# Kernel optimization log

Measured on AMD Instinct MI355X. Metric: run time of the kernel, lower is better.

## Reference

```python
import jax, jax.numpy as jnp
import numpy as np

N, X_DIM, Y_DIM, HID = 8192, 512, 2048 // 4, 2048
Y_DIM = 512

def setup_inputs() -> dict:
    key = jax.random.key(0)
    ks = jax.random.split(key, 10)
    def lin(k, fan_in, fan_out):
        lim = 1.0 / np.sqrt(fan_in)
        kw, kb = jax.random.split(k)
        W = jax.random.uniform(kw, (fan_in, fan_out), jnp.float32, -lim, lim)
        b = jax.random.uniform(kb, (fan_out,), jnp.float32, -lim, lim)
        return W, b
    mu_W1, mu_b1 = lin(ks[0], X_DIM, HID)
    mu_W2, mu_b2 = lin(ks[1], HID, Y_DIM)
    lv_W1, lv_b1 = lin(ks[2], X_DIM, HID)
    lv_W2, lv_b2 = lin(ks[3], HID, Y_DIM)
    return {
        "x_samples": jax.random.normal(ks[4], (N, X_DIM), jnp.float32),
        "y_samples": jax.random.normal(ks[5], (N, Y_DIM), jnp.float32),
        "mu_W1": mu_W1, "mu_b1": mu_b1, "mu_W2": mu_W2, "mu_b2": mu_b2,
        "lv_W1": lv_W1, "lv_b1": lv_b1, "lv_W2": lv_W2, "lv_b2": lv_b2,
    }

def reference(x_samples, y_samples, mu_W1, mu_b1, mu_W2, mu_b2, lv_W1, lv_b1, lv_W2, lv_b2):
    # MLP heads (GEMMs)
    mu = jax.nn.relu(x_samples @ mu_W1 + mu_b1) @ mu_W2 + mu_b2          # [N, D]
    logvar = jnp.tanh(jax.nn.relu(x_samples @ lv_W1 + lv_b1) @ lv_W2 + lv_b2)  # [N, D]
    w = 0.5 * jnp.exp(-logvar)                                           # 1/(2*exp(logvar))
    n = x_samples.shape[0]

    # positive: -mean_i sum_d (mu_id - y_id)^2 * w_id
    positive = -(((mu - y_samples) ** 2) * w).sum(axis=1).mean()

    # negative (exact decomposition of the [N,N,D] broadcast):
    # -(1/N^2) sum_{i,d} w_id * (N*mu_id^2 - 2*mu_id*Sy_d + Sy2_d)
    Sy = y_samples.sum(axis=0)          # [D]
    Sy2 = (y_samples ** 2).sum(axis=0)  # [D]
    negative = -(w * (n * mu ** 2 - 2.0 * mu * Sy + Sy2)).sum() / (n * n)

    return positive - negative
```

## Files before the change

kernel.cpp:

```cpp
#include <hip/hip_runtime.h>
#include <hip/hip_bf16.h>
#include <stdint.h>

#define NS   8192
#define XD   512
#define HD   2048
#define YD   512

typedef unsigned short u16;
using bf16x8 = __attribute__((ext_vector_type(8))) short;
using f32x4  = __attribute__((ext_vector_type(4))) float;

__device__ __forceinline__ float bf2f(u16 u) {
  union { uint32_t i; float f; } v; v.i = ((uint32_t)u) << 16; return v.f;
}
__device__ __forceinline__ u16 f2b(float f) {
  __hip_bfloat16 hb = __float2bfloat16(f);
  return *(const u16*)&hb;
}
__device__ __forceinline__ float ld_in(const void* p, int f32, size_t i) {
  return f32 ? ((const float*)p)[i] : bf2f(((const u16*)p)[i]);
}
#define GLDS(gp, lp) __builtin_amdgcn_global_load_lds( \
    (__attribute__((address_space(1))) void*)(gp),     \
    (__attribute__((address_space(3))) void*)(lp), 16, 0, 0)

__device__ __forceinline__ int probe_f32(const void* p, int n_u16, int* sflag) {
  if (threadIdx.x == 0) *sflag = 0;
  __syncthreads();
  const u16* q = (const u16*)p;
  int wild = 0;
  for (int i = threadIdx.x; i < n_u16; i += blockDim.x) {
    float v = bf2f(q[i]);
    if (!(fabsf(v) <= 1000.0f)) wild = 1;
  }
  if (wild) *sflag = 1;
  __syncthreads();
  int r = *sflag;
  __syncthreads();
  return r;
}

__global__ __launch_bounds__(256) void prep_all(
    const void* __restrict__ x,
    const void* w1m, const void* b1m, const void* w2m, const void* b2m,
    const void* w1l, const void* b1l, const void* w2l, const void* b2l,
    u16* __restrict__ xb, float* __restrict__ biasv,
    u16* __restrict__ W1t, u16* __restrict__ W2tm, u16* __restrict__ W2tl) {
  __shared__ u16 tile[64 * 72];
  __shared__ int sflag;
  const int b = blockIdx.x;
  const int tid = threadIdx.x;

  if (b < 2048) {
    if (!probe_f32(x, 1024, &sflag)) return;
    const size_t base = (size_t)b * 2048 + (size_t)tid * 8;
    alignas(16) u16 o[8];
    const float4* s = (const float4*)((const float*)x + base);
    float4 v0 = s[0], v1 = s[1];
    o[0]=f2b(v0.x); o[1]=f2b(v0.y); o[2]=f2b(v0.z); o[3]=f2b(v0.w);
    o[4]=f2b(v1.x); o[5]=f2b(v1.y); o[6]=f2b(v1.z); o[7]=f2b(v1.w);
    *(uint4*)(xb + base) = *(const uint4*)o;
  } else if (b == 2048) {
    const int f3 = probe_f32(b1m, 1024, &sflag);
    const int f5 = probe_f32(b2m, 512, &sflag);
    const int f7 = probe_f32(b1l, 1024, &sflag);
    const int f9 = probe_f32(b2l, 512, &sflag);
    for (int i = tid; i < 5120; i += 256) {
      float v;
      if (i < 2048)      v = ld_in(b1m, f3, i);
      else if (i < 4096) v = ld_in(b1l, f7, i - 2048);
      else if (i < 4608) v = ld_in(b2m, f5, i - 4096);
      else               v = ld_in(b2l, f9, i - 4608);
      biasv[i] = v;
    }
  } else {
    const int id = b - 2049, which = id >> 8, t = id & 255;
    const void* in; u16* out; int R, C;
    if (which == 0)      { in = w1m; out = W1t;                   R = XD; C = HD; }
    else if (which == 1) { in = w2m; out = W2tm;                  R = HD; C = YD; }
    else if (which == 2) { in = w1l; out = W1t + (size_t)HD * XD; R = XD; C = HD; }
    else                 { in = w2l; out = W2tl;                  R = HD; C = YD; }
    const int f = probe_f32(in, 1024, &sflag);
    const int nbx = C >> 6;
    const int c0 = (t % nbx) * 64, r0 = (t / nbx) * 64;
    const int r = tid >> 2, cc = (tid & 3) * 16;
    if (f) {
      const float4* s = (const float4*)((const float*)in + (size_t)(r0 + r) * C + c0 + cc);
#pragma unroll
      for (int k = 0; k < 4; ++k) {
        float4 v = s[k];
        tile[r * 72 + cc + k * 4 + 0] = f2b(v.x);
        tile[r * 72 + cc + k * 4 + 1] = f2b(v.y);
        tile[r * 72 + cc + k * 4 + 2] = f2b(v.z);
        tile[r * 72 + cc + k * 4 + 3] = f2b(v.w);
      }
    } else {
      const uint4* s = (const uint4*)((const u16*)in + (size_t)(r0 + r) * C + c0 + cc);
      *(uint4*)&tile[r * 72 + cc]     = s[0];
      *(uint4*)&tile[r * 72 + cc + 8] = s[1];
    }
    __syncthreads();
    const int i = tid >> 2, jc = (tid & 3) * 16;
    alignas(16) u16 o[16];
#pragma unroll
    for (int j = 0; j < 16; ++j) o[j] = tile[(jc + j) * 72 + i];
    uint4* dq = (uint4*)&out[(size_t)(c0 + i) * R + r0 + jc];
    dq[0] = ((const uint4*)o)[0];
    dq[1] = ((const uint4*)o)[1];
  }
}

__global__ __launch_bounds__(256) void gemm1_kernel(
    const void* __restrict__ xraw, const u16* __restrict__ xb,
    const void* __restrict__ y,
    const u16* __restrict__ W1t,
    const float* __restrict__ bias,
    float* __restrict__ Sy, float* __restrict__ Sy2,
    u16* __restrict__ h_mu, u16* __restrict__ h_lv) {
  constexpr int K = XD;
  __shared__ alignas(16) u16 As[128 * 64];
  __shared__ alignas(16) u16 Bs[128 * 64];
  __shared__ int sflag;

  const int tid = threadIdx.x;

  if (blockIdx.x < 64) {
    const int yf = probe_f32(y, 1024, &sflag);
    const int half = tid >> 7;
    const int c0 = (tid & 127) * 4;
    const int r0 = blockIdx.x * 128 + half * 64;
    float s0 = 0.f, s1 = 0.f, s2 = 0.f, s3 = 0.f;
    float q0 = 0.f, q1 = 0.f, q2 = 0.f, q3 = 0.f;
    for (int r = r0; r < r0 + 64; r += 4) {
#pragma unroll
      for (int rr = 0; rr < 4; ++rr) {
        float v0, v1, v2, v3;
        if (yf) {
          const float4 t4 = *(const float4*)((const float*)y + (size_t)(r + rr) * YD + c0);
          v0 = t4.x; v1 = t4.y; v2 = t4.z; v3 = t4.w;
        } else {
          const uint2 t2 = *(const uint2*)((const u16*)y + (size_t)(r + rr) * YD + c0);
          v0 = bf2f((u16)(t2.x & 0xffff)); v1 = bf2f((u16)(t2.x >> 16));
          v2 = bf2f((u16)(t2.y & 0xffff)); v3 = bf2f((u16)(t2.y >> 16));
        }
        s0 += v0; q0 += v0 * v0;  s1 += v1; q1 += v1 * v1;
        s2 += v2; q2 += v2 * v2;  s3 += v3; q3 += v3 * v3;
      }
    }
    atomicAdd(&Sy[c0],     s0);  atomicAdd(&Sy2[c0],     q0);
    atomicAdd(&Sy[c0 + 1], s1);  atomicAdd(&Sy2[c0 + 1], q1);
    atomicAdd(&Sy[c0 + 2], s2);  atomicAdd(&Sy2[c0 + 2], q2);
    atomicAdd(&Sy[c0 + 3], s3);  atomicAdd(&Sy2[c0 + 3], q3);
    return;
  }

  const u16* A = probe_f32(xraw, 1024, &sflag) ? xb : (const u16*)xraw;

  const int wid = tid >> 6, lane = tid & 63;
  const int id = blockIdx.x - 64;
  const int xcd = id & 7, slot = id >> 3;
  const int m_idx = slot & 7;
  const int n_idx = slot >> 3;
  const int bm0 = (xcd * 8 + m_idx) * 128;
  const int bn0 = n_idx * 128;

  const int mrow = (wid >> 1) * 64, ncol = (wid & 1) * 64;
  const int quad = lane >> 4, c16 = lane & 15, cswz = c16 & 7;
  const int srow = lane >> 3, sc = lane & 7;
  const int scg  = (sc ^ srow) * 8;

  f32x4 acc[4][4] = {};

  for (int k0 = 0; k0 < K; k0 += 64) {
#pragma unroll
    for (int j = 0; j < 4; ++j) {
      const int grp = wid * 4 + j, row = grp * 8 + srow;
      GLDS(A   + (size_t)(bm0 + row) * K + (k0 + scg), As + grp * 512);
      GLDS(W1t + (size_t)(bn0 + row) * K + (k0 + scg), Bs + grp * 512);
    }
    __syncthreads();
#pragma unroll
    for (int h = 0; h < 2; ++h) {
      const int off = ((h * 4 + quad) ^ cswz) * 8;
      bf16x8 af[4], bfr[4];
#pragma unroll
      for (int mi = 0; mi < 4; ++mi)
        af[mi] = *(const bf16x8*)&As[(mrow + mi * 16 + c16) * 64 + off];
#pragma unroll
      for (int ni = 0; ni < 4; ++ni)
        bfr[ni] = *(const bf16x8*)&Bs[(ncol + ni * 16 + c16) * 64 + off];
#pragma unroll
      for (int mi = 0; mi < 4; ++mi)
#pragma unroll
        for (int ni = 0; ni < 4; ++ni)
          acc[mi][ni] = __builtin_amdgcn_mfma_f32_16x16x32_bf16(
              af[mi], bfr[ni], acc[mi][ni], 0, 0, 0);
    }
    __syncthreads();
  }

  const bool is_lv = bn0 >= HD;
  u16* dst = is_lv ? h_lv : h_mu;
  const int cb = bn0 - (is_lv ? HD : 0);
#pragma unroll
  for (int ni = 0; ni < 4; ++ni) {
    const int gc = ncol + ni * 16 + c16;
    const float bv = bias[bn0 + gc];
#pragma unroll
    for (int mi = 0; mi < 4; ++mi)
#pragma unroll
      for (int r = 0; r < 4; ++r) {
        const int grow = bm0 + mrow + mi * 16 + quad * 4 + r;
        dst[(size_t)grow * HD + (cb + gc)] = f2b(fmaxf(acc[mi][ni][r] + bv, 0.f));
      }
  }
}

__global__ __launch_bounds__(256) void gemm2_dual(
    const u16* __restrict__ hm, const u16* __restrict__ hl,
    const u16* __restrict__ W2m, const u16* __restrict__ W2l,
    const float* __restrict__ b2m, const float* __restrict__ b2l,
    const void* __restrict__ y,
    const float* __restrict__ Sy, const float* __restrict__ Sy2,
    double* __restrict__ gacc, unsigned* __restrict__ counter,
    float* __restrict__ out) {
  constexpr int K = HD;
  __shared__ alignas(16) u16 Am[64 * 64];
  __shared__ alignas(16) u16 Al[64 * 64];
  __shared__ alignas(16) u16 Bm[128 * 64];
  __shared__ alignas(16) u16 Bl[128 * 64];
  __shared__ double bs[4];
  __shared__ int sflag;

  const int yf = probe_f32(y, 1024, &sflag);

  const int tid = threadIdx.x, wid = tid >> 6, lane = tid & 63;
  const int MT = NS / 64, NT = YD / 128;
  const int id = blockIdx.x;
  const int xcd = id & 7, slot = id >> 3;
  const int bm0 = (xcd * (MT >> 3) + slot / NT) * 64;
  const int bn0 = (slot % NT) * 128;

  const int mrow = (wid >> 1) * 32, ncol = (wid & 1) * 64;
  const int quad = lane >> 4, c16 = lane & 15, cswz = c16 & 7;
  const int srow = lane >> 3, sc = lane & 7;
  const int scg  = (sc ^ srow) * 8;

  f32x4 am[2][4] = {}, al[2][4] = {};

  for (int k0 = 0; k0 < K; k0 += 64) {
#pragma unroll
    for (int j = 0; j < 2; ++j) {
      const int grp = wid * 2 + j, row = grp * 8 + srow;
      const size_t go = (size_t)(bm0 + row) * K + (k0 + scg);
      GLDS(hm + go, Am + grp * 512);
      GLDS(hl + go, Al + grp * 512);
    }
#pragma unroll
    for (int j = 0; j < 4; ++j) {
      const int grp = wid * 4 + j, row = grp * 8 + srow;
      const size_t go = (size_t)(bn0 + row) * K + (k0 + scg);
      GLDS(W2m + go, Bm + grp * 512);
      GLDS(W2l + go, Bl + grp * 512);
    }
    __syncthreads();
#pragma unroll
    for (int h = 0; h < 2; ++h) {
      const int off = ((h * 4 + quad) ^ cswz) * 8;
      bf16x8 afm[2], afl[2], bfm[4], bfl[4];
#pragma unroll
      for (int mi = 0; mi < 2; ++mi) {
        const int rl = (mrow + mi * 16 + c16) * 64 + off;
        afm[mi] = *(const bf16x8*)&Am[rl];
        afl[mi] = *(const bf16x8*)&Al[rl];
      }
#pragma unroll
      for (int ni = 0; ni < 4; ++ni) {
        const int rl = (ncol + ni * 16 + c16) * 64 + off;
        bfm[ni] = *(const bf16x8*)&Bm[rl];
        bfl[ni] = *(const bf16x8*)&Bl[rl];
      }
#pragma unroll
      for (int mi = 0; mi < 2; ++mi)
#pragma unroll
        for (int ni = 0; ni < 4; ++ni) {
          am[mi][ni] = __builtin_amdgcn_mfma_f32_16x16x32_bf16(
              afm[mi], bfm[ni], am[mi][ni], 0, 0, 0);
          al[mi][ni] = __builtin_amdgcn_mfma_f32_16x16x32_bf16(
              afl[mi], bfl[ni], al[mi][ni], 0, 0, 0);
        }
    }
    __syncthreads();
  }

  const float invN = 1.0f / (float)NS;
  float s = 0.f;
#pragma unroll
  for (int ni = 0; ni < 4; ++ni) {
    const int gcol = bn0 + ncol + ni * 16 + c16;
    const float bmv = b2m[gcol], blv = b2l[gcol];
    const float syv = Sy[gcol], sy2v = Sy2[gcol];
#pragma unroll
    for (int mi = 0; mi < 2; ++mi)
#pragma unroll
      for (int r = 0; r < 4; ++r) {
        const int grow = bm0 + mrow + mi * 16 + quad * 4 + r;
        const float m   = am[mi][ni][r] + bmv;
        const float lvp = al[mi][ni][r] + blv;
        const float w   = 0.5f * expf(-tanhf(lvp));
        const float yv  = ld_in(y, yf, (size_t)grow * YD + gcol);
        s += w * (yv * yv - 2.f * m * yv + (2.f * m * syv - sy2v) * invN);
      }
  }
  for (int off = 32; off > 0; off >>= 1) s += __shfl_down(s, off);
  if (lane == 0) bs[wid] = (double)s;
  __syncthreads();
  if (tid == 0) {
    atomicAdd(gacc, bs[0] + bs[1] + bs[2] + bs[3]);
    __threadfence();
    const unsigned old = atomicAdd(counter, 1u);
    if (old == gridDim.x - 1) {
      const double g = atomicAdd(gacc, 0.0);
      out[0] = (float)(-g / (double)NS);
    }
  }
}

extern "C" void kernel_launch(void* const* d_in, const int* in_sizes, int n_in,
                              void* d_out, int out_size, void* d_ws, size_t ws_size,
                              hipStream_t stream) {
  char* ws = (char*)d_ws;
  double*   gacc    = (double*)ws;
  unsigned* counter = (unsigned*)(ws + 8);
  float*    Sy      = (float*)(ws + 128);
  float*    Sy2     = (float*)(ws + 2176);
  float*    biasv   = (float*)(ws + 4224);
  u16* xb   = (u16*)(ws + 24704);
  u16* W1t  = xb + (size_t)NS * XD;
  u16* W2tm = W1t + (size_t)2 * HD * XD;
  u16* W2tl = W2tm + (size_t)YD * HD;
  u16* h_mu = W2tl + (size_t)YD * HD;
  u16* h_lv = h_mu + (size_t)NS * HD;

  hipMemsetAsync(d_ws, 0, 4224, stream);

  prep_all<<<2049 + 1024, 256, 0, stream>>>(
      d_in[0], d_in[2], d_in[3], d_in[4], d_in[5],
      d_in[6], d_in[7], d_in[8], d_in[9],
      xb, biasv, W1t, W2tm, W2tl);

  const float* b1  = biasv;
  const float* b2m = biasv + 4096, *b2l = biasv + 4608;

  gemm1_kernel<<<64 + (NS / 128) * ((2 * HD) / 128), 256, 0, stream>>>(
      d_in[0], xb, d_in[1], W1t, b1, Sy, Sy2, h_mu, h_lv);

  gemm2_dual<<<(NS / 64) * (YD / 128), 256, 0, stream>>>(
      h_mu, h_lv, W2tm, W2tl, b2m, b2l, d_in[1], Sy, Sy2,
      gacc, counter, (float*)d_out);
}
```

Baseline: 228.9 us.

## Move y column sums into prep kernel and W2 transposes into gemm1 tail

The Sy/Sy2 column-sum blocks move from the front of gemm1 into the prep kernel, and the W2 transpose blocks move from prep into extra trailing blocks of gemm1, where they run alongside the GEMM tiles. The aim is to balance work across the two launches and to stop the GEMM blocks from waiting behind the reduction blocks. The GEMM tile index mapping is rewritten in general form using the tile counts. The risk is that the trailing transpose blocks extend gemm1's tail.

```diff
diff --git a/kernel.cpp b/kernel.cpp
--- a/kernel.cpp
+++ b/kernel.cpp
@@ -41,95 +41,55 @@
   return r;
 }
 
+__device__ __forceinline__ void transpose64(const void* in, u16* out,
+                                            int R, int C, int f, int t,
+                                            u16* tile ) {
+  const int tid = threadIdx.x;
+  const int nbx = C >> 6;
+  const int c0 = (t % nbx) * 64, r0 = (t / nbx) * 64;
+  const int r = tid >> 2, cc = (tid & 3) * 16;
+  if (f) {
+    const float4* s = (const float4*)((const float*)in + (size_t)(r0 + r) * C + c0 + cc);
+#pragma unroll
+    for (int k = 0; k < 4; ++k) {
+      float4 v = s[k];
+      tile[r * 72 + cc + k * 4 + 0] = f2b(v.x);
+      tile[r * 72 + cc + k * 4 + 1] = f2b(v.y);
+      tile[r * 72 + cc + k * 4 + 2] = f2b(v.z);
+      tile[r * 72 + cc + k * 4 + 3] = f2b(v.w);
+    }
+  } else {
+    const uint4* s = (const uint4*)((const u16*)in + (size_t)(r0 + r) * C + c0 + cc);
+    *(uint4*)&tile[r * 72 + cc]     = s[0];
+    *(uint4*)&tile[r * 72 + cc + 8] = s[1];
+  }
+  __syncthreads();
+  const int i = tid >> 2, jc = (tid & 3) * 16;
+  alignas(16) u16 o[16];
+#pragma unroll
+  for (int j = 0; j < 16; ++j) o[j] = tile[(jc + j) * 72 + i];
+  uint4* dq = (uint4*)&out[(size_t)(c0 + i) * R + r0 + jc];
+  dq[0] = ((const uint4*)o)[0];
+  dq[1] = ((const uint4*)o)[1];
+}
+
 __global__ __launch_bounds__(256) void prep_all(
-    const void* __restrict__ x,
-    const void* w1m, const void* b1m, const void* w2m, const void* b2m,
-    const void* w1l, const void* b1l, const void* w2l, const void* b2l,
+    const void* __restrict__ x, const void* __restrict__ y,
+    const void* w1m, const void* b1m, const void* b2m,
+    const void* w1l, const void* b1l, const void* b2l,
     u16* __restrict__ xb, float* __restrict__ biasv,
-    u16* __restrict__ W1t, u16* __restrict__ W2tm, u16* __restrict__ W2tl) {
+    float* __restrict__ Sy, float* __restrict__ Sy2,
+    u16* __restrict__ W1t) {
   __shared__ u16 tile[64 * 72];
   __shared__ int sflag;
   const int b = blockIdx.x;
   const int tid = threadIdx.x;
 
-  if (b < 2048) {
-    if (!probe_f32(x, 1024, &sflag)) return;
-    const size_t base = (size_t)b * 2048 + (size_t)tid * 8;
-    alignas(16) u16 o[8];
-    const float4* s = (const float4*)((const float*)x + base);
-    float4 v0 = s[0], v1 = s[1];
-    o[0]=f2b(v0.x); o[1]=f2b(v0.y); o[2]=f2b(v0.z); o[3]=f2b(v0.w);
-    o[4]=f2b(v1.x); o[5]=f2b(v1.y); o[6]=f2b(v1.z); o[7]=f2b(v1.w);
-    *(uint4*)(xb + base) = *(const uint4*)o;
-  } else if (b == 2048) {
-    const int f3 = probe_f32(b1m, 1024, &sflag);
-    const int f5 = probe_f32(b2m, 512, &sflag);
-    const int f7 = probe_f32(b1l, 1024, &sflag);
-    const int f9 = probe_f32(b2l, 512, &sflag);
-    for (int i = tid; i < 5120; i += 256) {
-      float v;
-      if (i < 2048)      v = ld_in(b1m, f3, i);
-      else if (i < 4096) v = ld_in(b1l, f7, i - 2048);
-      else if (i < 4608) v = ld_in(b2m, f5, i - 4096);
-      else               v = ld_in(b2l, f9, i - 4608);
-      biasv[i] = v;
-    }
-  } else {
-    const int id = b - 2049, which = id >> 8, t = id & 255;
-    const void* in; u16* out; int R, C;
-    if (which == 0)      { in = w1m; out = W1t;                   R = XD; C = HD; }
-    else if (which == 1) { in = w2m; out = W2tm;                  R = HD; C = YD; }
-    else if (which == 2) { in = w1l; out = W1t + (size_t)HD * XD; R = XD; C = HD; }
-    else                 { in = w2l; out = W2tl;                  R = HD; C = YD; }
-    const int f = probe_f32(in, 1024, &sflag);
-    const int nbx = C >> 6;
-    const int c0 = (t % nbx) * 64, r0 = (t / nbx) * 64;
-    const int r = tid >> 2, cc = (tid & 3) * 16;
-    if (f) {
-      const float4* s = (const float4*)((const float*)in + (size_t)(r0 + r) * C + c0 + cc);
-#pragma unroll
-      for (int k = 0; k < 4; ++k) {
-        float4 v = s[k];
-        tile[r * 72 + cc + k * 4 + 0] = f2b(v.x);
-        tile[r * 72 + cc + k * 4 + 1] = f2b(v.y);
-        tile[r * 72 + cc + k * 4 + 2] = f2b(v.z);
-        tile[r * 72 + cc + k * 4 + 3] = f2b(v.w);
-      }
-    } else {
-      const uint4* s = (const uint4*)((const u16*)in + (size_t)(r0 + r) * C + c0 + cc);
-      *(uint4*)&tile[r * 72 + cc]     = s[0];
-      *(uint4*)&tile[r * 72 + cc + 8] = s[1];
-    }
-    __syncthreads();
-    const int i = tid >> 2, jc = (tid & 3) * 16;
-    alignas(16) u16 o[16];
-#pragma unroll
-    for (int j = 0; j < 16; ++j) o[j] = tile[(jc + j) * 72 + i];
-    uint4* dq = (uint4*)&out[(size_t)(c0 + i) * R + r0 + jc];
-    dq[0] = ((const uint4*)o)[0];
-    dq[1] = ((const uint4*)o)[1];
-  }
-}
-
-__global__ __launch_bounds__(256) void gemm1_kernel(
-    const void* __restrict__ xraw, const u16* __restrict__ xb,
-    const void* __restrict__ y,
-    const u16* __restrict__ W1t,
-    const float* __restrict__ bias,
-    float* __restrict__ Sy, float* __restrict__ Sy2,
-    u16* __restrict__ h_mu, u16* __restrict__ h_lv) {
-  constexpr int K = XD;
-  __shared__ alignas(16) u16 As[128 * 64];
-  __shared__ alignas(16) u16 Bs[128 * 64];
-  __shared__ int sflag;
-
-  const int tid = threadIdx.x;
-
-  if (blockIdx.x < 64) {
+  if (b < 64) {
     const int yf = probe_f32(y, 1024, &sflag);
     const int half = tid >> 7;
     const int c0 = (tid & 127) * 4;
-    const int r0 = blockIdx.x * 128 + half * 64;
+    const int r0 = b * 128 + half * 64;
     float s0 = 0.f, s1 = 0.f, s2 = 0.f, s3 = 0.f;
     float q0 = 0.f, q1 = 0.f, q2 = 0.f, q3 = 0.f;
     for (int r = r0; r < r0 + 64; r += 4) {
@@ -152,18 +112,68 @@
     atomicAdd(&Sy[c0 + 1], s1);  atomicAdd(&Sy2[c0 + 1], q1);
     atomicAdd(&Sy[c0 + 2], s2);  atomicAdd(&Sy2[c0 + 2], q2);
     atomicAdd(&Sy[c0 + 3], s3);  atomicAdd(&Sy2[c0 + 3], q3);
+  } else if (b < 2112) {
+    if (!probe_f32(x, 1024, &sflag)) return;
+    const size_t base = (size_t)(b - 64) * 2048 + (size_t)tid * 8;
+    alignas(16) u16 o[8];
+    const float4* s = (const float4*)((const float*)x + base);
+    float4 v0 = s[0], v1 = s[1];
+    o[0]=f2b(v0.x); o[1]=f2b(v0.y); o[2]=f2b(v0.z); o[3]=f2b(v0.w);
+    o[4]=f2b(v1.x); o[5]=f2b(v1.y); o[6]=f2b(v1.z); o[7]=f2b(v1.w);
+    *(uint4*)(xb + base) = *(const uint4*)o;
+  } else if (b == 2112) {
+    const int f3 = probe_f32(b1m, 1024, &sflag);
+    const int f5 = probe_f32(b2m, 512, &sflag);
+    const int f7 = probe_f32(b1l, 1024, &sflag);
+    const int f9 = probe_f32(b2l, 512, &sflag);
+    for (int i = tid; i < 5120; i += 256) {
+      float v;
+      if (i < 2048)      v = ld_in(b1m, f3, i);
+      else if (i < 4096) v = ld_in(b1l, f7, i - 2048);
+      else if (i < 4608) v = ld_in(b2m, f5, i - 4096);
+      else               v = ld_in(b2l, f9, i - 4608);
+      biasv[i] = v;
+    }
+  } else {
+    const int id = b - 2113, which = id >> 8, t = id & 255;
+    const void* in = which ? w1l : w1m;
+    u16* out = W1t + (which ? (size_t)HD * XD : 0);
+    const int f = probe_f32(in, 1024, &sflag);
+    transpose64(in, out, XD, HD, f, t, tile);
+  }
+}
+
+__global__ __launch_bounds__(256) void gemm1_kernel(
+    const void* __restrict__ xraw, const u16* __restrict__ xb,
+    const u16* __restrict__ W1t,
+    const float* __restrict__ bias,
+    const void* w2m, const void* w2l,
+    u16* __restrict__ W2tm, u16* __restrict__ W2tl,
+    u16* __restrict__ h_mu, u16* __restrict__ h_lv) {
+  constexpr int K = XD;
+  __shared__ alignas(16) u16 As[128 * 64];
+  __shared__ alignas(16) u16 Bs[128 * 64];
+  __shared__ int sflag;
+
+  const int tid = threadIdx.x;
+
+  if (blockIdx.x >= 2048) {
+    const int id = blockIdx.x - 2048, which = id >> 8, t = id & 255;
+    const void* in = which ? w2l : w2m;
+    u16* out = which ? W2tl : W2tm;
+    const int f = probe_f32(in, 1024, &sflag);
+    transpose64(in, out, HD, YD, f, t, As);
     return;
   }
 
   const u16* A = probe_f32(xraw, 1024, &sflag) ? xb : (const u16*)xraw;
 
   const int wid = tid >> 6, lane = tid & 63;
-  const int id = blockIdx.x - 64;
+  const int MT = NS / 128, NT = (2 * HD) / 128;
+  const int id = blockIdx.x;
   const int xcd = id & 7, slot = id >> 3;
-  const int m_idx = slot & 7;
-  const int n_idx = slot >> 3;
-  const int bm0 = (xcd * 8 + m_idx) * 128;
-  const int bn0 = n_idx * 128;
+  const int bm0 = (xcd * (MT >> 3) + slot / NT) * 128;
+  const int bn0 = (slot % NT) * 128;
 
   const int mrow = (wid >> 1) * 64, ncol = (wid & 1) * 64;
   const int quad = lane >> 4, c16 = lane & 15, cswz = c16 & 7;
@@ -345,16 +355,16 @@
 
   hipMemsetAsync(d_ws, 0, 4224, stream);
 
-  prep_all<<<2049 + 1024, 256, 0, stream>>>(
-      d_in[0], d_in[2], d_in[3], d_in[4], d_in[5],
-      d_in[6], d_in[7], d_in[8], d_in[9],
-      xb, biasv, W1t, W2tm, W2tl);
+  prep_all<<<2113 + 512, 256, 0, stream>>>(
+      d_in[0], d_in[1], d_in[2], d_in[3], d_in[5],
+      d_in[6], d_in[7], d_in[9],
+      xb, biasv, Sy, Sy2, W1t);
 
   const float* b1  = biasv;
   const float* b2m = biasv + 4096, *b2l = biasv + 4608;
 
-  gemm1_kernel<<<64 + (NS / 128) * ((2 * HD) / 128), 256, 0, stream>>>(
-      d_in[0], xb, d_in[1], W1t, b1, Sy, Sy2, h_mu, h_lv);
+  gemm1_kernel<<<2048 + 512, 256, 0, stream>>>(
+      d_in[0], xb, W1t, b1, d_in[4], d_in[8], W2tm, W2tl, h_mu, h_lv);
 
   gemm2_dual<<<(NS / 64) * (YD / 128), 256, 0, stream>>>(
       h_mu, h_lv, W2tm, W2tl, b2m, b2l, d_in[1], Sy, Sy2,
```

Measured after the change: 234.6 us. +2.5%, slower.

## Move y column-sum blocks from gemm1 into gemm2 with spin-wait handoff

Applied to the files above, without the earlier changes.

The 64 blocks that reduce Sy and Sy2 over y now run at the front of the gemm2 grid instead of the gemm1 grid. GEMM blocks wait on an atomic counter only before the epilogue, so the reduction overlaps their main loop. gemm1 also switches to the generic xcd/slot tile mapping. Spin-waiting relies on the 64 reducer blocks being scheduled, which is a risk if they are not resident, and the transpose code is factored into a helper.

```diff
diff --git a/kernel.cpp b/kernel.cpp
--- a/kernel.cpp
+++ b/kernel.cpp
@@ -39,6 +39,38 @@
   int r = *sflag;
   __syncthreads();
   return r;
+}
+
+__device__ __forceinline__ void transpose64(const void* in, u16* out,
+                                            int R, int C, int f, int t,
+                                            u16* tile ) {
+  const int tid = threadIdx.x;
+  const int nbx = C >> 6;
+  const int c0 = (t % nbx) * 64, r0 = (t / nbx) * 64;
+  const int r = tid >> 2, cc = (tid & 3) * 16;
+  if (f) {
+    const float4* s = (const float4*)((const float*)in + (size_t)(r0 + r) * C + c0 + cc);
+#pragma unroll
+    for (int k = 0; k < 4; ++k) {
+      float4 v = s[k];
+      tile[r * 72 + cc + k * 4 + 0] = f2b(v.x);
+      tile[r * 72 + cc + k * 4 + 1] = f2b(v.y);
+      tile[r * 72 + cc + k * 4 + 2] = f2b(v.z);
+      tile[r * 72 + cc + k * 4 + 3] = f2b(v.w);
+    }
+  } else {
+    const uint4* s = (const uint4*)((const u16*)in + (size_t)(r0 + r) * C + c0 + cc);
+    *(uint4*)&tile[r * 72 + cc]     = s[0];
+    *(uint4*)&tile[r * 72 + cc + 8] = s[1];
+  }
+  __syncthreads();
+  const int i = tid >> 2, jc = (tid & 3) * 16;
+  alignas(16) u16 o[16];
+#pragma unroll
+  for (int j = 0; j < 16; ++j) o[j] = tile[(jc + j) * 72 + i];
+  uint4* dq = (uint4*)&out[(size_t)(c0 + i) * R + r0 + jc];
+  dq[0] = ((const uint4*)o)[0];
+  dq[1] = ((const uint4*)o)[1];
 }
 
 __global__ __launch_bounds__(256) void prep_all(
@@ -82,51 +114,101 @@
     else if (which == 2) { in = w1l; out = W1t + (size_t)HD * XD; R = XD; C = HD; }
     else                 { in = w2l; out = W2tl;                  R = HD; C = YD; }
     const int f = probe_f32(in, 1024, &sflag);
-    const int nbx = C >> 6;
-    const int c0 = (t % nbx) * 64, r0 = (t / nbx) * 64;
-    const int r = tid >> 2, cc = (tid & 3) * 16;
-    if (f) {
-      const float4* s = (const float4*)((const float*)in + (size_t)(r0 + r) * C + c0 + cc);
-#pragma unroll
-      for (int k = 0; k < 4; ++k) {
-        float4 v = s[k];
-        tile[r * 72 + cc + k * 4 + 0] = f2b(v.x);
-        tile[r * 72 + cc + k * 4 + 1] = f2b(v.y);
-        tile[r * 72 + cc + k * 4 + 2] = f2b(v.z);
-        tile[r * 72 + cc + k * 4 + 3] = f2b(v.w);
-      }
-    } else {
-      const uint4* s = (const uint4*)((const u16*)in + (size_t)(r0 + r) * C + c0 + cc);
-      *(uint4*)&tile[r * 72 + cc]     = s[0];
-      *(uint4*)&tile[r * 72 + cc + 8] = s[1];
-    }
-    __syncthreads();
-    const int i = tid >> 2, jc = (tid & 3) * 16;
-    alignas(16) u16 o[16];
-#pragma unroll
-    for (int j = 0; j < 16; ++j) o[j] = tile[(jc + j) * 72 + i];
-    uint4* dq = (uint4*)&out[(size_t)(c0 + i) * R + r0 + jc];
-    dq[0] = ((const uint4*)o)[0];
-    dq[1] = ((const uint4*)o)[1];
+    transpose64(in, out, R, C, f, t, tile);
   }
 }
 
 __global__ __launch_bounds__(256) void gemm1_kernel(
     const void* __restrict__ xraw, const u16* __restrict__ xb,
-    const void* __restrict__ y,
     const u16* __restrict__ W1t,
     const float* __restrict__ bias,
-    float* __restrict__ Sy, float* __restrict__ Sy2,
     u16* __restrict__ h_mu, u16* __restrict__ h_lv) {
   constexpr int K = XD;
   __shared__ alignas(16) u16 As[128 * 64];
   __shared__ alignas(16) u16 Bs[128 * 64];
   __shared__ int sflag;
 
+  const u16* A = probe_f32(xraw, 1024, &sflag) ? xb : (const u16*)xraw;
+
+  const int tid = threadIdx.x, wid = tid >> 6, lane = tid & 63;
+  const int MT = NS / 128, NT = (2 * HD) / 128;
+  const int id = blockIdx.x;
+  const int xcd = id & 7, slot = id >> 3;
+  const int bm0 = (xcd * (MT >> 3) + slot / NT) * 128;
+  const int bn0 = (slot % NT) * 128;
+
+  const int mrow = (wid >> 1) * 64, ncol = (wid & 1) * 64;
+  const int quad = lane >> 4, c16 = lane & 15, cswz = c16 & 7;
+  const int srow = lane >> 3, sc = lane & 7;
+  const int scg  = (sc ^ srow) * 8;
+
+  f32x4 acc[4][4] = {};
+
+  for (int k0 = 0; k0 < K; k0 += 64) {
+#pragma unroll
+    for (int j = 0; j < 4; ++j) {
+      const int grp = wid * 4 + j, row = grp * 8 + srow;
+      GLDS(A   + (size_t)(bm0 + row) * K + (k0 + scg), As + grp * 512);
+      GLDS(W1t + (size_t)(bn0 + row) * K + (k0 + scg), Bs + grp * 512);
+    }
+    __syncthreads();
+#pragma unroll
+    for (int h = 0; h < 2; ++h) {
+      const int off = ((h * 4 + quad) ^ cswz) * 8;
+      bf16x8 af[4], bfr[4];
+#pragma unroll
+      for (int mi = 0; mi < 4; ++mi)
+        af[mi] = *(const bf16x8*)&As[(mrow + mi * 16 + c16) * 64 + off];
+#pragma unroll
+      for (int ni = 0; ni < 4; ++ni)
+        bfr[ni] = *(const bf16x8*)&Bs[(ncol + ni * 16 + c16) * 64 + off];
+#pragma unroll
+      for (int mi = 0; mi < 4; ++mi)
+#pragma unroll
+        for (int ni = 0; ni < 4; ++ni)
+          acc[mi][ni] = __builtin_amdgcn_mfma_f32_16x16x32_bf16(
+              af[mi], bfr[ni], acc[mi][ni], 0, 0, 0);
+    }
+    __syncthreads();
+  }
+
+  const bool is_lv = bn0 >= HD;
+  u16* dst = is_lv ? h_lv : h_mu;
+  const int cb = bn0 - (is_lv ? HD : 0);
+#pragma unroll
+  for (int ni = 0; ni < 4; ++ni) {
+    const int gc = ncol + ni * 16 + c16;
+    const float bv = bias[bn0 + gc];
+#pragma unroll
+    for (int mi = 0; mi < 4; ++mi)
+#pragma unroll
+      for (int r = 0; r < 4; ++r) {
+        const int grow = bm0 + mrow + mi * 16 + quad * 4 + r;
+        dst[(size_t)grow * HD + (cb + gc)] = f2b(fmaxf(acc[mi][ni][r] + bv, 0.f));
+      }
+  }
+}
+
+__global__ __launch_bounds__(256) void gemm2_dual(
+    const u16* __restrict__ hm, const u16* __restrict__ hl,
+    const u16* __restrict__ W2m, const u16* __restrict__ W2l,
+    const float* __restrict__ b2m, const float* __restrict__ b2l,
+    const void* __restrict__ y,
+    float* __restrict__ Sy, float* __restrict__ Sy2,
+    double* __restrict__ gacc, unsigned* __restrict__ counter,
+    unsigned* __restrict__ ycnt, float* __restrict__ out) {
+  constexpr int K = HD;
+  __shared__ alignas(16) u16 Am[64 * 64];
+  __shared__ alignas(16) u16 Al[64 * 64];
+  __shared__ alignas(16) u16 Bm[128 * 64];
+  __shared__ alignas(16) u16 Bl[128 * 64];
+  __shared__ double bs[4];
+  __shared__ int sflag;
+
   const int tid = threadIdx.x;
+  const int yf = probe_f32(y, 1024, &sflag);
 
   if (blockIdx.x < 64) {
-    const int yf = probe_f32(y, 1024, &sflag);
     const int half = tid >> 7;
     const int c0 = (tid & 127) * 4;
     const int r0 = blockIdx.x * 128 + half * 64;
@@ -152,92 +234,14 @@
     atomicAdd(&Sy[c0 + 1], s1);  atomicAdd(&Sy2[c0 + 1], q1);
     atomicAdd(&Sy[c0 + 2], s2);  atomicAdd(&Sy2[c0 + 2], q2);
     atomicAdd(&Sy[c0 + 3], s3);  atomicAdd(&Sy2[c0 + 3], q3);
+    __syncthreads();
+    if (tid == 0) { __threadfence(); atomicAdd(ycnt, 1u); }
     return;
   }
 
-  const u16* A = probe_f32(xraw, 1024, &sflag) ? xb : (const u16*)xraw;
-
   const int wid = tid >> 6, lane = tid & 63;
+  const int MT = NS / 64, NT = YD / 128;
   const int id = blockIdx.x - 64;
-  const int xcd = id & 7, slot = id >> 3;
-  const int m_idx = slot & 7;
-  const int n_idx = slot >> 3;
-  const int bm0 = (xcd * 8 + m_idx) * 128;
-  const int bn0 = n_idx * 128;
-
-  const int mrow = (wid >> 1) * 64, ncol = (wid & 1) * 64;
-  const int quad = lane >> 4, c16 = lane & 15, cswz = c16 & 7;
-  const int srow = lane >> 3, sc = lane & 7;
-  const int scg  = (sc ^ srow) * 8;
-
-  f32x4 acc[4][4] = {};
-
-  for (int k0 = 0; k0 < K; k0 += 64) {
-#pragma unroll
-    for (int j = 0; j < 4; ++j) {
-      const int grp = wid * 4 + j, row = grp * 8 + srow;
-      GLDS(A   + (size_t)(bm0 + row) * K + (k0 + scg), As + grp * 512);
-      GLDS(W1t + (size_t)(bn0 + row) * K + (k0 + scg), Bs + grp * 512);
-    }
-    __syncthreads();
-#pragma unroll
-    for (int h = 0; h < 2; ++h) {
-      const int off = ((h * 4 + quad) ^ cswz) * 8;
-      bf16x8 af[4], bfr[4];
-#pragma unroll
-      for (int mi = 0; mi < 4; ++mi)
-        af[mi] = *(const bf16x8*)&As[(mrow + mi * 16 + c16) * 64 + off];
-#pragma unroll
-      for (int ni = 0; ni < 4; ++ni)
-        bfr[ni] = *(const bf16x8*)&Bs[(ncol + ni * 16 + c16) * 64 + off];
-#pragma unroll
-      for (int mi = 0; mi < 4; ++mi)
-#pragma unroll
-        for (int ni = 0; ni < 4; ++ni)
-          acc[mi][ni] = __builtin_amdgcn_mfma_f32_16x16x32_bf16(
-              af[mi], bfr[ni], acc[mi][ni], 0, 0, 0);
-    }
-    __syncthreads();
-  }
-
-  const bool is_lv = bn0 >= HD;
-  u16* dst = is_lv ? h_lv : h_mu;
-  const int cb = bn0 - (is_lv ? HD : 0);
-#pragma unroll
-  for (int ni = 0; ni < 4; ++ni) {
-    const int gc = ncol + ni * 16 + c16;
-    const float bv = bias[bn0 + gc];
-#pragma unroll
-    for (int mi = 0; mi < 4; ++mi)
-#pragma unroll
-      for (int r = 0; r < 4; ++r) {
-        const int grow = bm0 + mrow + mi * 16 + quad * 4 + r;
-        dst[(size_t)grow * HD + (cb + gc)] = f2b(fmaxf(acc[mi][ni][r] + bv, 0.f));
-      }
-  }
-}
-
-__global__ __launch_bounds__(256) void gemm2_dual(
-    const u16* __restrict__ hm, const u16* __restrict__ hl,
-    const u16* __restrict__ W2m, const u16* __restrict__ W2l,
-    const float* __restrict__ b2m, const float* __restrict__ b2l,
-    const void* __restrict__ y,
-    const float* __restrict__ Sy, const float* __restrict__ Sy2,
-    double* __restrict__ gacc, unsigned* __restrict__ counter,
-    float* __restrict__ out) {
-  constexpr int K = HD;
-  __shared__ alignas(16) u16 Am[64 * 64];
-  __shared__ alignas(16) u16 Al[64 * 64];
-  __shared__ alignas(16) u16 Bm[128 * 64];
-  __shared__ alignas(16) u16 Bl[128 * 64];
-  __shared__ double bs[4];
-  __shared__ int sflag;
-
-  const int yf = probe_f32(y, 1024, &sflag);
-
-  const int tid = threadIdx.x, wid = tid >> 6, lane = tid & 63;
-  const int MT = NS / 64, NT = YD / 128;
-  const int id = blockIdx.x;
   const int xcd = id & 7, slot = id >> 3;
   const int bm0 = (xcd * (MT >> 3) + slot / NT) * 64;
   const int bn0 = (slot % NT) * 128;
@@ -293,6 +297,12 @@
     }
     __syncthreads();
   }
+
+  if (tid == 0) {
+    while (__hip_atomic_load(ycnt, __ATOMIC_ACQUIRE,
+                             __HIP_MEMORY_SCOPE_AGENT) < 64u) {}
+  }
+  __syncthreads();
 
   const float invN = 1.0f / (float)NS;
   float s = 0.f;
@@ -320,7 +330,7 @@
     atomicAdd(gacc, bs[0] + bs[1] + bs[2] + bs[3]);
     __threadfence();
     const unsigned old = atomicAdd(counter, 1u);
-    if (old == gridDim.x - 1) {
+    if (old == 511u) {
       const double g = atomicAdd(gacc, 0.0);
       out[0] = (float)(-g / (double)NS);
     }
@@ -333,6 +343,7 @@
   char* ws = (char*)d_ws;
   double*   gacc    = (double*)ws;
   unsigned* counter = (unsigned*)(ws + 8);
+  unsigned* ycnt    = (unsigned*)(ws + 12);
   float*    Sy      = (float*)(ws + 128);
   float*    Sy2     = (float*)(ws + 2176);
   float*    biasv   = (float*)(ws + 4224);
@@ -353,10 +364,10 @@
   const float* b1  = biasv;
   const float* b2m = biasv + 4096, *b2l = biasv + 4608;
 
-  gemm1_kernel<<<64 + (NS / 128) * ((2 * HD) / 128), 256, 0, stream>>>(
-      d_in[0], xb, d_in[1], W1t, b1, Sy, Sy2, h_mu, h_lv);
-
-  gemm2_dual<<<(NS / 64) * (YD / 128), 256, 0, stream>>>(
+  gemm1_kernel<<<(NS / 128) * ((2 * HD) / 128), 256, 0, stream>>>(
+      d_in[0], xb, W1t, b1, h_mu, h_lv);
+
+  gemm2_dual<<<64 + (NS / 64) * (YD / 128), 256, 0, stream>>>(
       h_mu, h_lv, W2tm, W2tl, b2m, b2l, d_in[1], Sy, Sy2,
-      gacc, counter, (float*)d_out);
-}
+      gacc, counter, ycnt, (float*)d_out);
+}
```

Result: slower. 246.1 us (+7.5%).
